# Optimization experiments

Measured on AMD Instinct MI355X. Metric: run time of the kernel, lower is better.

## Reference

```python
import jax, jax.numpy as jnp
import numpy as np

T, IO, H, M = 8192, 32, 256, 4  # timesteps, io_width, hidden_width, max ponder steps
EPS = 0.01  # ACT halting epsilon


def setup_inputs() -> dict:
    key = jax.random.key(0)
    ks = jax.random.split(key, 8)
    sc = 0.05
    return {
        "x": jax.random.normal(ks[0], (T, IO), jnp.float32),
        "h0": jnp.zeros((H,), jnp.float32),                       # act1_h initial state
        "Wp": jax.random.normal(ks[1], (H, IO), jnp.float32) * sc,  # input_processing Linear
        "bp": jnp.zeros((H,), jnp.float32),
        "Wx": jax.random.normal(ks[2], (H, H + 1), jnp.float32) * sc,  # ACT cell input weights (+1 first-step flag)
        "Ws": jax.random.normal(ks[3], (H, H), jnp.float32) * sc,      # ACT cell recurrent weights
        "b": jnp.zeros((H,), jnp.float32),
        "wh": jax.random.normal(ks[4], (H,), jnp.float32) * sc,        # halting unit
        "bh": jnp.float32(1.0),
        "Wo": jax.random.normal(ks[5], (IO, H), jnp.float32) * sc,     # ACT output projection
        "bo": jnp.zeros((IO,), jnp.float32),
    }


def reference(x, h0, Wp, bp, Wx, Ws, b, wh, bh, Wo, bo):
    # Faithful translation: per-timestep loop (lax.scan) over the sequence; each step
    # runs input_processing then an ACT (Graves) ponder loop with max M=4 steps.
    # io_noise is identity in eval mode. attention_beam_width=1 => line == current point.
    T_ = x.shape[0]

    def step(carry, x_t):
        h, pc = carry
        lin1 = Wp @ x_t + bp  # [H]
        s = h
        cum = jnp.float32(0.0)
        acc_s = jnp.zeros_like(h)
        acc_y = jnp.zeros_like(bo)
        n_up = jnp.float32(0.0)
        rem = jnp.float32(0.0)
        still = jnp.bool_(True)
        for n in range(M):  # fixed small ponder loop, masked ACT halting
            flag = jnp.full((1,), 1.0 if n == 0 else 0.0, lin1.dtype)
            inp = jnp.concatenate([lin1, flag])  # [H+1]
            s = jnp.tanh(Wx @ inp + Ws @ s + b)
            p = jax.nn.sigmoid(wh @ s + bh)
            halt = (cum + p > 1.0 - EPS) | (n == M - 1)
            w = jnp.where(still, jnp.where(halt, 1.0 - cum, p), 0.0)
            acc_s = acc_s + w * s
            acc_y = acc_y + w * (Wo @ s + bo)
            rem = rem + jnp.where(still & halt, 1.0 - cum, 0.0)
            n_up = n_up + jnp.where(still, 1.0, 0.0)
            cum = cum + w
            still = still & jnp.logical_not(halt)
        ponder = n_up + rem  # N(t) + R(t)
        pc = (pc + ponder) / jnp.float32(T_)  # matches the in-loop division in the original forward
        return (acc_s, pc), acc_y

    (_, pc), ys = jax.lax.scan(step, (h0, jnp.float32(0.0)), x)
    return ys, pc
```

## Files before the change

kernel.cpp:

```cpp
#include <hip/hip_runtime.h>


#define T_  8192
#define IO_ 32
#define H_  256

typedef __attribute__((ext_vector_type(8))) __bf16 bf16x8;
typedef __attribute__((ext_vector_type(4))) float  f32x4;

__device__ __forceinline__ unsigned short f2bf(float f) {
    union { float f; unsigned int u; } v;
    v.f = f;
    unsigned int u = v.u;
    u += 0x7FFFu + ((u >> 16) & 1u);
    return (unsigned short)(u >> 16);
}

template<int CTRL>
__device__ __forceinline__ float dpp_addf(float x) {
    int xi = __builtin_bit_cast(int, x);
    int d = __builtin_amdgcn_update_dpp(xi, xi, CTRL, 0xF, 0xF, false);
    return x + __builtin_bit_cast(float, d);
}

__device__ __forceinline__ float wave_sum63(float x) {
    x = dpp_addf<0xB1>(x);
    x = dpp_addf<0x4E>(x);
    x = dpp_addf<0x124>(x);
    x = dpp_addf<0x128>(x);
    x = dpp_addf<0x142>(x);
    x = dpp_addf<0x143>(x);
    return x;
}

__global__ void k_prep(const float* __restrict__ Wx,
                       const float* __restrict__ Wp,
                       const float* __restrict__ bp,
                       const float* __restrict__ b,
                       float* __restrict__ WxpT, float* __restrict__ cvec) {
    int h = blockIdx.x;
    int t = threadIdx.x;
    __shared__ float wxrow[H_];
    for (int j = t; j < H_; j += 64) wxrow[j] = Wx[h * (H_ + 1) + j];
    __syncthreads();
    if (t < IO_) {
        float acc = 0.0f;
        for (int j = 0; j < H_; ++j) acc += wxrow[j] * Wp[j * IO_ + t];
        WxpT[t * H_ + h] = acc;
    } else if (t == IO_) {
        float acc = b[h];
        for (int j = 0; j < H_; ++j) acc += wxrow[j] * bp[j];
        cvec[h] = acc;
    }
}

__global__ void k_u(const float* __restrict__ x,
                    const float* __restrict__ WxpT,
                    const float* __restrict__ cvec,
                    float* __restrict__ U) {
    int t0 = blockIdx.x * 8;
    int tid = threadIdx.x;
    __shared__ float xsf[8 * IO_];
    xsf[tid] = x[(size_t)t0 * IO_ + tid];
    __syncthreads();
    int h = tid;
    float base = cvec[h];
    for (int tt = 0; tt < 8; ++tt) {
        float acc = base;
        #pragma unroll
        for (int io = 0; io < IO_; ++io)
            acc += WxpT[io * H_ + h] * xsf[tt * IO_ + io];
        U[(size_t)(t0 + tt) * H_ + h] = acc;
    }
}

__global__ __launch_bounds__(256, 1) void act_chain(
    const float* __restrict__ Ws,
    const float* __restrict__ Wx,
    const float* __restrict__ wh,
    const float* __restrict__ bh1,
    const float* __restrict__ h0,
    float* __restrict__ UAcc,
    float* __restrict__ cumArr,
    float* __restrict__ pc_out)
{
    __shared__ __align__(16) unsigned short sbuf[H_];
    __shared__ __align__(16) float ybuf[H_];
    __shared__ __align__(16) float plds[4];

    const int tid  = threadIdx.x;
    const int w    = tid >> 6;
    const int l    = tid & 63;
    const int quad = l >> 4;
    const int col  = l & 15;
    const int L    = tid;

    bf16x8 af[4][8];
    #pragma unroll
    for (int b = 0; b < 4; ++b) {
        const float* row = Ws + (size_t)(w * 64 + b * 16 + col) * H_;
        #pragma unroll
        for (int c = 0; c < 8; ++c) {
            union { unsigned short u[8]; bf16x8 v; } tmp;
            #pragma unroll
            for (int j = 0; j < 8; ++j)
                tmp.u[j] = f2bf(row[c * 32 + quad * 8 + j]);
            af[b][c] = tmp.v;
        }
    }

    const float wlL = Wx[(size_t)L * (H_ + 1) + H_];
    const float whL = wh[L];
    const float bhf = bh1[0];
    const float thresh = 1.0f - 0.01f;
    const float L2E  = 1.4426950408889634f;
    const float L2E2 = 2.8853900817779268f;

    sbuf[L] = f2bf(h0[L]);
    __syncthreads();
    float Wsh;
    {
        f32x4 C[4] = {{0,0,0,0},{0,0,0,0},{0,0,0,0},{0,0,0,0}};
        #pragma unroll
        for (int c = 0; c < 8; ++c) {
            bf16x8 bf = *reinterpret_cast<const bf16x8*>(
                (const char*)sbuf + c * 64 + quad * 16);
            #pragma unroll
            for (int b = 0; b < 4; ++b)
                C[b] = __builtin_amdgcn_mfma_f32_16x16x32_bf16(af[b][c], bf, C[b], 0, 0, 0);
        }
        if (col == 0) {
            #pragma unroll
            for (int b = 0; b < 4; ++b)
                *(f32x4*)(&ybuf[w * 64 + b * 16 + quad * 4]) = C[b];
        }
        __syncthreads();
        Wsh = ybuf[L];
    }

    float u = UAcc[L];
    float s, pc = 0.0f;
    {
        float a = u + wlL + Wsh;
        float e = __builtin_amdgcn_exp2f(a * L2E2);
        s = __builtin_fmaf(-2.0f, __builtin_amdgcn_rcpf(e + 1.0f), 1.0f);
        float part = wave_sum63(whL * s);
        if (l == 63) plds[w] = part;
        sbuf[L] = f2bf(s);
    }
    float acc = 0.0f, Wacc = 0.0f, cum = 0.0f, nup = 1.0f;
    __syncthreads();

    #pragma unroll 1
    for (int t = 0; t < T_; ++t) {
        float un = (t + 1 < T_) ? UAcc[(size_t)(t + 1) * H_ + L] : 0.0f;

        #pragma unroll 1
        for (int k = 1; k <= 4; ++k) {
            f32x4 C[4] = {{0,0,0,0},{0,0,0,0},{0,0,0,0},{0,0,0,0}};
            #pragma unroll
            for (int c = 0; c < 8; ++c) {
                bf16x8 bf = *reinterpret_cast<const bf16x8*>(
                    (const char*)sbuf + c * 64 + quad * 16);
                #pragma unroll
                for (int b = 0; b < 4; ++b)
                    C[b] = __builtin_amdgcn_mfma_f32_16x16x32_bf16(af[b][c], bf, C[b], 0, 0, 0);
            }

            f32x4 pv = *(const f32x4*)plds;
            float dot = (pv[0] + pv[1]) + (pv[2] + pv[3]);
            float p = __builtin_amdgcn_rcpf(
                1.0f + __builtin_amdgcn_exp2f(-(dot + bhf) * L2E));
            bool halt = (cum + p > thresh) || (k == 4);
            float hw = 1.0f - cum;
            float wn = halt ? hw : p;
            acc = __builtin_fmaf(wn, s, acc);
            cum += wn;

            if (col == 0) {
                #pragma unroll
                for (int b = 0; b < 4; ++b)
                    *(f32x4*)(&ybuf[w * 64 + b * 16 + quad * 4]) = C[b];
            }
            __syncthreads();

            float yL = ybuf[L];
            Wacc = __builtin_fmaf(wn, yL, Wacc);

            if (halt) {
                pc = (pc + nup + hw) * (1.0f / (float)T_);
                UAcc[(size_t)t * H_ + L] = acc;
                if (tid == 0) cumArr[t] = cum;
                float a = un + wlL + Wacc;
                float e = __builtin_amdgcn_exp2f(a * L2E2);
                s = __builtin_fmaf(-2.0f, __builtin_amdgcn_rcpf(e + 1.0f), 1.0f);
                float part = wave_sum63(whL * s);
                if (l == 63) plds[w] = part;
                sbuf[L] = f2bf(s);
                u = un;
                acc = 0.0f; Wacc = 0.0f; cum = 0.0f; nup = 1.0f;
                __syncthreads();
                break;
            } else {
                float a = u + yL;
                float e = __builtin_amdgcn_exp2f(a * L2E2);
                s = __builtin_fmaf(-2.0f, __builtin_amdgcn_rcpf(e + 1.0f), 1.0f);
                float part = wave_sum63(whL * s);
                if (l == 63) plds[w] = part;
                sbuf[L] = f2bf(s);
                nup += 1.0f;
                __syncthreads();
            }
        }
    }
    if (tid == 0) pc_out[0] = pc;
}

__global__ void k_out(const float* __restrict__ AccS,
                      const float* __restrict__ Wo,
                      const float* __restrict__ bo,
                      const float* __restrict__ cumArr,
                      float* __restrict__ ys) {
    int t0 = blockIdx.x * 8;
    int tid = threadIdx.x;
    __shared__ float wo[IO_ * 257];
    __shared__ float as[8 * 260];
    for (int i = tid; i < IO_ * H_; i += 256) {
        int o = i / H_, h = i % H_;
        wo[o * 257 + h] = Wo[i];
    }
    for (int i = tid; i < 8 * H_; i += 256) {
        int tt = i / H_, h = i % H_;
        as[tt * 260 + h] = AccS[(size_t)t0 * H_ + i];
    }
    __syncthreads();
    int tt = tid >> 5, o = tid & 31;
    float acc = cumArr[t0 + tt] * bo[o];
    #pragma unroll 4
    for (int h = 0; h < H_; ++h) acc += wo[o * 257 + h] * as[tt * 260 + h];
    ys[(size_t)(t0 + tt) * IO_ + o] = acc;
}

extern "C" void kernel_launch(void* const* d_in, const int* in_sizes, int n_in,
                              void* d_out, int out_size, void* d_ws, size_t ws_size,
                              hipStream_t stream) {
    const float* x  = (const float*)d_in[0];
    const float* h0 = (const float*)d_in[1];
    const float* Wp = (const float*)d_in[2];
    const float* bp = (const float*)d_in[3];
    const float* Wx = (const float*)d_in[4];
    const float* Ws = (const float*)d_in[5];
    const float* b  = (const float*)d_in[6];
    const float* wh = (const float*)d_in[7];
    const float* bh = (const float*)d_in[8];
    const float* Wo = (const float*)d_in[9];
    const float* bo = (const float*)d_in[10];
    float* out = (float*)d_out;

    char* ws = (char*)d_ws;
    float* WxpT = (float*)ws;
    float* cvec = (float*)(ws + 32768);
    float* cumA = (float*)(ws + 33792);
    float* UAcc = (float*)(ws + 66560);

    k_prep<<<H_, 64, 0, stream>>>(Wx, Wp, bp, b, WxpT, cvec);
    k_u<<<T_ / 8, 256, 0, stream>>>(x, WxpT, cvec, UAcc);
    act_chain<<<1, 256, 0, stream>>>(Ws, Wx, wh, bh, h0, UAcc, cumA,
                                     out + (size_t)T_ * IO_);
    k_out<<<T_ / 8, 256, 0, stream>>>(UAcc, Wo, bo, cumA, out);
}
```

Measured before the change: 13.75 ms.

## Keep MFMA outputs in registers, double-buffer state, and batch UAcc I/O

The sequential ACT chain now has each lane own four hidden rows taken straight from its MFMA accumulators. This removes the ybuf LDS round trip and halves the barriers per ponder step to one, using double-buffered sbuf/plds. Next-step inputs are prefetched as float4 in groups of eight timesteps, and accumulated states and cum values are written back once per group. The cost is redundant tanh work on non-owner lanes and higher register pressure.

```diff
diff --git a/kernel.cpp b/kernel.cpp
--- a/kernel.cpp
+++ b/kernel.cpp
@@ -84,16 +84,16 @@
     float* __restrict__ cumArr,
     float* __restrict__ pc_out)
 {
-    __shared__ __align__(16) unsigned short sbuf[H_];
-    __shared__ __align__(16) float ybuf[H_];
-    __shared__ __align__(16) float plds[4];
+    __shared__ __align__(16) unsigned short sbuf[2][H_];
+    __shared__ __align__(16) float plds[2][4];
 
     const int tid  = threadIdx.x;
     const int w    = tid >> 6;
     const int l    = tid & 63;
     const int quad = l >> 4;
     const int col  = l & 15;
-    const int L    = tid;
+    const bool owner = (col < 4);
+    const int R0 = w * 64 + (owner ? col : 0) * 16 + quad * 4;
 
     bf16x8 af[4][8];
     #pragma unroll
@@ -109,108 +109,164 @@
         }
     }
 
-    const float wlL = Wx[(size_t)L * (H_ + 1) + H_];
-    const float whL = wh[L];
+    float wl4[4], whv4[4];
+    #pragma unroll
+    for (int r = 0; r < 4; ++r) {
+        wl4[r]  = Wx[(size_t)(R0 + r) * (H_ + 1) + H_];
+        whv4[r] = owner ? wh[R0 + r] : 0.0f;
+    }
     const float bhf = bh1[0];
     const float thresh = 1.0f - 0.01f;
     const float L2E  = 1.4426950408889634f;
     const float L2E2 = 2.8853900817779268f;
 
-    sbuf[L] = f2bf(h0[L]);
+    sbuf[0][tid] = f2bf(h0[tid]);
     __syncthreads();
-    float Wsh;
+
+    float sn4[4], ucur4[4], acc4[4], Wac4[4];
+    float cum = 0.0f, nup = 1.0f, pc = 0.0f;
+    int   P = 1;
+
     {
-        f32x4 C[4] = {{0,0,0,0},{0,0,0,0},{0,0,0,0},{0,0,0,0}};
+        f32x4 C0 = {0,0,0,0}, C1 = C0, C2 = C0, C3 = C0;
         #pragma unroll
         for (int c = 0; c < 8; ++c) {
             bf16x8 bf = *reinterpret_cast<const bf16x8*>(
-                (const char*)sbuf + c * 64 + quad * 16);
+                (const char*)&sbuf[0][0] + c * 64 + quad * 16);
+            C0 = __builtin_amdgcn_mfma_f32_16x16x32_bf16(af[0][c], bf, C0, 0, 0, 0);
+            C1 = __builtin_amdgcn_mfma_f32_16x16x32_bf16(af[1][c], bf, C1, 0, 0, 0);
+            C2 = __builtin_amdgcn_mfma_f32_16x16x32_bf16(af[2][c], bf, C2, 0, 0, 0);
+            C3 = __builtin_amdgcn_mfma_f32_16x16x32_bf16(af[3][c], bf, C3, 0, 0, 0);
+        }
+        float4 u0 = *(const float4*)(UAcc + R0);
+        ucur4[0] = u0.x; ucur4[1] = u0.y; ucur4[2] = u0.z; ucur4[3] = u0.w;
+        float part = 0.0f;
+        #pragma unroll
+        for (int r = 0; r < 4; ++r) {
+            float y = (col == 0) ? C0[r] : (col == 1) ? C1[r]
+                    : (col == 2) ? C2[r] : C3[r];
+            float a = ucur4[r] + wl4[r] + y;
+            float e = __builtin_amdgcn_exp2f(a * L2E2);
+            sn4[r] = __builtin_fmaf(-2.0f, __builtin_amdgcn_rcpf(e + 1.0f), 1.0f);
+            part = __builtin_fmaf(whv4[r], sn4[r], part);
+            acc4[r] = 0.0f; Wac4[r] = 0.0f;
+        }
+        if (owner) {
+            uint2 pk;
+            pk.x = (unsigned)f2bf(sn4[0]) | ((unsigned)f2bf(sn4[1]) << 16);
+            pk.y = (unsigned)f2bf(sn4[2]) | ((unsigned)f2bf(sn4[3]) << 16);
+            *(uint2*)(&sbuf[1][R0]) = pk;
+        }
+        part = wave_sum63(part);
+        if (l == 63) plds[1][w] = part;
+        __syncthreads();
+    }
+
+    #pragma unroll 1
+    for (int g = 0; g < T_ / 8; ++g) {
+        float4 un[8];
+        #pragma unroll
+        for (int j = 0; j < 8; ++j) {
+            int tn = g * 8 + 1 + j;
+            if (tn > T_ - 1) tn = T_ - 1;
+            un[j] = *(const float4*)(UAcc + (size_t)tn * H_ + R0);
+        }
+        float4 av[8];
+        float  cu8[8];
+
+        #pragma unroll
+        for (int j = 0; j < 8; ++j) {
+            #pragma unroll 1
+            for (int k = 1; k <= 4; ++k) {
+                f32x4 pv = *(const f32x4*)(&plds[P][0]);
+                f32x4 C0 = {0,0,0,0}, C1 = C0, C2 = C0, C3 = C0;
+                #pragma unroll
+                for (int c = 0; c < 8; ++c) {
+                    bf16x8 bf = *reinterpret_cast<const bf16x8*>(
+                        (const char*)&sbuf[P][0] + c * 64 + quad * 16);
+                    C0 = __builtin_amdgcn_mfma_f32_16x16x32_bf16(af[0][c], bf, C0, 0, 0, 0);
+                    C1 = __builtin_amdgcn_mfma_f32_16x16x32_bf16(af[1][c], bf, C1, 0, 0, 0);
+                    C2 = __builtin_amdgcn_mfma_f32_16x16x32_bf16(af[2][c], bf, C2, 0, 0, 0);
+                    C3 = __builtin_amdgcn_mfma_f32_16x16x32_bf16(af[3][c], bf, C3, 0, 0, 0);
+                }
+                float y4[4];
+                #pragma unroll
+                for (int r = 0; r < 4; ++r)
+                    y4[r] = (col == 0) ? C0[r] : (col == 1) ? C1[r]
+                          : (col == 2) ? C2[r] : C3[r];
+
+                float dot = (pv[0] + pv[1]) + (pv[2] + pv[3]);
+                float p = __builtin_amdgcn_rcpf(
+                    1.0f + __builtin_amdgcn_exp2f(-(dot + bhf) * L2E));
+                bool halt = (cum + p > thresh) || (k == 4);
+                float hw = 1.0f - cum;
+                float wn = halt ? hw : p;
+                #pragma unroll
+                for (int r = 0; r < 4; ++r) {
+                    acc4[r] = __builtin_fmaf(wn, sn4[r], acc4[r]);
+                    Wac4[r] = __builtin_fmaf(wn, y4[r], Wac4[r]);
+                }
+                cum += wn;
+
+                if (halt) {
+                    pc = (pc + nup + hw) * (1.0f / (float)T_);
+                    av[j]  = make_float4(acc4[0], acc4[1], acc4[2], acc4[3]);
+                    cu8[j] = cum;
+                    const float* up = (const float*)&un[j];
+                    float part = 0.0f;
+                    #pragma unroll
+                    for (int r = 0; r < 4; ++r) {
+                        float a = up[r] + wl4[r] + Wac4[r];
+                        float e = __builtin_amdgcn_exp2f(a * L2E2);
+                        sn4[r] = __builtin_fmaf(-2.0f, __builtin_amdgcn_rcpf(e + 1.0f), 1.0f);
+                        part = __builtin_fmaf(whv4[r], sn4[r], part);
+                        ucur4[r] = up[r];
+                        acc4[r] = 0.0f; Wac4[r] = 0.0f;
+                    }
+                    if (owner) {
+                        uint2 pk;
+                        pk.x = (unsigned)f2bf(sn4[0]) | ((unsigned)f2bf(sn4[1]) << 16);
+                        pk.y = (unsigned)f2bf(sn4[2]) | ((unsigned)f2bf(sn4[3]) << 16);
+                        *(uint2*)(&sbuf[P ^ 1][R0]) = pk;
+                    }
+                    part = wave_sum63(part);
+                    if (l == 63) plds[P ^ 1][w] = part;
+                    cum = 0.0f; nup = 1.0f;
+                    P ^= 1;
+                    __syncthreads();
+                    break;
+                } else {
+                    float part = 0.0f;
+                    #pragma unroll
+                    for (int r = 0; r < 4; ++r) {
+                        float a = ucur4[r] + y4[r];
+                        float e = __builtin_amdgcn_exp2f(a * L2E2);
+                        sn4[r] = __builtin_fmaf(-2.0f, __builtin_amdgcn_rcpf(e + 1.0f), 1.0f);
+                        part = __builtin_fmaf(whv4[r], sn4[r], part);
+                    }
+                    if (owner) {
+                        uint2 pk;
+                        pk.x = (unsigned)f2bf(sn4[0]) | ((unsigned)f2bf(sn4[1]) << 16);
+                        pk.y = (unsigned)f2bf(sn4[2]) | ((unsigned)f2bf(sn4[3]) << 16);
+                        *(uint2*)(&sbuf[P ^ 1][R0]) = pk;
+                    }
+                    part = wave_sum63(part);
+                    if (l == 63) plds[P ^ 1][w] = part;
+                    nup += 1.0f;
+                    P ^= 1;
+                    __syncthreads();
+                }
+            }
+        }
+
+        if (owner) {
             #pragma unroll
-            for (int b = 0; b < 4; ++b)
-                C[b] = __builtin_amdgcn_mfma_f32_16x16x32_bf16(af[b][c], bf, C[b], 0, 0, 0);
-        }
-        if (col == 0) {
+            for (int j = 0; j < 8; ++j)
+                *(float4*)(UAcc + (size_t)(g * 8 + j) * H_ + R0) = av[j];
+        }
+        if (tid == 0) {
             #pragma unroll
-            for (int b = 0; b < 4; ++b)
-                *(f32x4*)(&ybuf[w * 64 + b * 16 + quad * 4]) = C[b];
-        }
-        __syncthreads();
-        Wsh = ybuf[L];
-    }
-
-    float u = UAcc[L];
-    float s, pc = 0.0f;
-    {
-        float a = u + wlL + Wsh;
-        float e = __builtin_amdgcn_exp2f(a * L2E2);
-        s = __builtin_fmaf(-2.0f, __builtin_amdgcn_rcpf(e + 1.0f), 1.0f);
-        float part = wave_sum63(whL * s);
-        if (l == 63) plds[w] = part;
-        sbuf[L] = f2bf(s);
-    }
-    float acc = 0.0f, Wacc = 0.0f, cum = 0.0f, nup = 1.0f;
-    __syncthreads();
-
-    #pragma unroll 1
-    for (int t = 0; t < T_; ++t) {
-        float un = (t + 1 < T_) ? UAcc[(size_t)(t + 1) * H_ + L] : 0.0f;
-
-        #pragma unroll 1
-        for (int k = 1; k <= 4; ++k) {
-            f32x4 C[4] = {{0,0,0,0},{0,0,0,0},{0,0,0,0},{0,0,0,0}};
-            #pragma unroll
-            for (int c = 0; c < 8; ++c) {
-                bf16x8 bf = *reinterpret_cast<const bf16x8*>(
-                    (const char*)sbuf + c * 64 + quad * 16);
-                #pragma unroll
-                for (int b = 0; b < 4; ++b)
-                    C[b] = __builtin_amdgcn_mfma_f32_16x16x32_bf16(af[b][c], bf, C[b], 0, 0, 0);
-            }
-
-            f32x4 pv = *(const f32x4*)plds;
-            float dot = (pv[0] + pv[1]) + (pv[2] + pv[3]);
-            float p = __builtin_amdgcn_rcpf(
-                1.0f + __builtin_amdgcn_exp2f(-(dot + bhf) * L2E));
-            bool halt = (cum + p > thresh) || (k == 4);
-            float hw = 1.0f - cum;
-            float wn = halt ? hw : p;
-            acc = __builtin_fmaf(wn, s, acc);
-            cum += wn;
-
-            if (col == 0) {
-                #pragma unroll
-                for (int b = 0; b < 4; ++b)
-                    *(f32x4*)(&ybuf[w * 64 + b * 16 + quad * 4]) = C[b];
-            }
-            __syncthreads();
-
-            float yL = ybuf[L];
-            Wacc = __builtin_fmaf(wn, yL, Wacc);
-
-            if (halt) {
-                pc = (pc + nup + hw) * (1.0f / (float)T_);
-                UAcc[(size_t)t * H_ + L] = acc;
-                if (tid == 0) cumArr[t] = cum;
-                float a = un + wlL + Wacc;
-                float e = __builtin_amdgcn_exp2f(a * L2E2);
-                s = __builtin_fmaf(-2.0f, __builtin_amdgcn_rcpf(e + 1.0f), 1.0f);
-                float part = wave_sum63(whL * s);
-                if (l == 63) plds[w] = part;
-                sbuf[L] = f2bf(s);
-                u = un;
-                acc = 0.0f; Wacc = 0.0f; cum = 0.0f; nup = 1.0f;
-                __syncthreads();
-                break;
-            } else {
-                float a = u + yL;
-                float e = __builtin_amdgcn_exp2f(a * L2E2);
-                s = __builtin_fmaf(-2.0f, __builtin_amdgcn_rcpf(e + 1.0f), 1.0f);
-                float part = wave_sum63(whL * s);
-                if (l == 63) plds[w] = part;
-                sbuf[L] = f2bf(s);
-                nup += 1.0f;
-                __syncthreads();
-            }
+            for (int j = 0; j < 8; ++j) cumArr[g * 8 + j] = cu8[j];
         }
     }
     if (tid == 0) pc_out[0] = pc;
```

After: 16.06 ms. 16.8% more time.
